# Optimization experiments

Measured on AMD Instinct MI355X. Metric: run time of the kernel, lower is better.

## Reference

```python
import jax, jax.numpy as jnp
import numpy as np

H = 128          # hidden
L = 4            # num PNA layers
NG = 32          # graphs in the batch
OUT = 12
N_NODES = 30000
N_EDGES = 480000
IN_NODE = 64
IN_EDGE = 16
EPS_BN = 1e-5
EPS_STD = 1e-5
# deg histogram torch.tensor([1,2,3,4,5,6]): cnt_i nodes have degree i
_cnt = np.arange(1.0, 7.0)
AVG_LOG = float((np.log(np.arange(6) + 1.0) * _cnt).sum() / _cnt.sum())


def _lin(k, fan_in, fan_out):
    return jax.random.normal(k, (fan_in, fan_out), jnp.float32) * 0.05


def setup_inputs() -> dict:
    key = jax.random.key(0)
    ks = jax.random.split(key, 16)
    d = {}
    d["x"] = jax.random.normal(ks[0], (N_NODES, IN_NODE), jnp.float32)
    d["edge_attr"] = jax.random.normal(ks[1], (N_EDGES, IN_EDGE), jnp.float32)
    d["edge_index"] = jax.random.randint(ks[2], (2, N_EDGES), 0, N_NODES)
    d["batch"] = jnp.sort(jax.random.randint(ks[3], (N_NODES,), 0, NG))
    d["node_emb_W"] = _lin(ks[4], IN_NODE, H)
    d["node_emb_b"] = jnp.zeros((H,), jnp.float32)
    d["edge_emb_W"] = _lin(ks[5], IN_EDGE, H)
    d["edge_emb_b"] = jnp.zeros((H,), jnp.float32)
    kl = jax.random.split(ks[6], 4 * L)
    d["edge_enc_W"] = jnp.stack([_lin(kl[i], H, H) for i in range(L)])
    d["edge_enc_b"] = jnp.zeros((L, H), jnp.float32)
    d["pre_W"] = jnp.stack([_lin(kl[L + i], 3 * H, H) for i in range(L)])
    d["pre_b"] = jnp.zeros((L, H), jnp.float32)
    d["post_W"] = jnp.stack([_lin(kl[2 * L + i], 13 * H, H) for i in range(L)])
    d["post_b"] = jnp.zeros((L, H), jnp.float32)
    d["lin_W"] = jnp.stack([_lin(kl[3 * L + i], H, H) for i in range(L)])
    d["lin_b"] = jnp.zeros((L, H), jnp.float32)
    d["bn_gamma"] = jnp.ones((L, H), jnp.float32)
    d["bn_beta"] = jnp.zeros((L, H), jnp.float32)
    d["head1_W"] = _lin(ks[7], H, H // 2)
    d["head1_b"] = jnp.zeros((H // 2,), jnp.float32)
    d["head2_W"] = _lin(ks[8], H // 2, OUT)
    d["head2_b"] = jnp.zeros((OUT,), jnp.float32)
    return d


def _pna_layer(x, e, src, dst, eW, eb, pW, pb, oW, ob, lW, lb):
    n = x.shape[0]
    ee = e @ eW + eb                                      # edge encoder [E, H]
    h = jnp.concatenate([x[dst], x[src], ee], axis=-1)    # (x_i, x_j, e) [E, 3H]
    m = h @ pW + pb                                       # pre-nn messages [E, H]
    ones = jnp.ones((m.shape[0],), m.dtype)
    deg = jax.ops.segment_sum(ones, dst, num_segments=n)  # in-degree [N]
    degc = jnp.maximum(deg, 1.0)[:, None]
    has = (deg > 0.0)[:, None]
    mean = jax.ops.segment_sum(m, dst, num_segments=n) / degc
    mn = jnp.where(has, jax.ops.segment_min(m, dst, num_segments=n), 0.0)
    mx = jnp.where(has, jax.ops.segment_max(m, dst, num_segments=n), 0.0)
    mean_sq = jax.ops.segment_sum(m * m, dst, num_segments=n) / degc
    std = jnp.sqrt(jax.nn.relu(mean_sq - mean * mean) + EPS_STD)
    agg = jnp.concatenate([mean, mn, mx, std], axis=-1)   # aggregators [N, 4H]
    amp = jnp.log(degc + 1.0) / AVG_LOG                   # amplification scale
    out = jnp.concatenate([agg, agg * amp, agg / amp], axis=-1)  # id/amp/atten [N, 12H]
    out = jnp.concatenate([x, out], axis=-1) @ oW + ob    # post-nn [N, H]
    return out @ lW + lb                                  # final lin


def reference(x, edge_index, batch, edge_attr, node_emb_W, node_emb_b,
              edge_emb_W, edge_emb_b, edge_enc_W, edge_enc_b, pre_W, pre_b,
              post_W, post_b, lin_W, lin_b, bn_gamma, bn_beta,
              head1_W, head1_b, head2_W, head2_b):
    src, dst = edge_index[0], edge_index[1]
    h = x @ node_emb_W + node_emb_b
    e = edge_attr @ edge_emb_W + edge_emb_b
    for l in range(L):
        h = _pna_layer(h, e, src, dst, edge_enc_W[l], edge_enc_b[l],
                       pre_W[l], pre_b[l], post_W[l], post_b[l],
                       lin_W[l], lin_b[l])
        mu = h.mean(axis=0)
        var = h.var(axis=0)  # biased, as BatchNorm training-mode normalization
        h = (h - mu) / jnp.sqrt(var + EPS_BN) * bn_gamma[l] + bn_beta[l]
        h = jax.nn.relu(h)   # dropout == identity (eval mode reference)
    g = jax.ops.segment_sum(h, batch, num_segments=NG)   # global_add_pool [NG, H]
    z = jax.nn.relu(g @ head1_W + head1_b)
    return z @ head2_W + head2_b
```

## Files before the change

kernel.cpp:

```cpp
#include <hip/hip_runtime.h>
#include <hip/hip_bf16.h>
#include <math.h>

#define NN 30000
#define NE 480000
#define NLAYER 4
#define NGR 32
#define NOUT 12
#define EPS_BN 1e-5f
#define EPS_STD 1e-5f
#define AVG_LOG 1.3821454785305053f
#define MB_GRID 235
#define MB2 469

typedef unsigned short ushort_t;
typedef __bf16 bf16x8 __attribute__((ext_vector_type(8)));
typedef float floatx4 __attribute__((ext_vector_type(4)));

__device__ __forceinline__ float bfu(ushort_t u){
  union { unsigned int ui; float f; } c; c.ui = ((unsigned int)u) << 16; return c.f;
}
__device__ __forceinline__ ushort_t f2bf(float f){
  union { float f; unsigned int u; } c; c.f = f;
  unsigned int lsb = (c.u >> 16) & 1u;
  c.u += 0x7FFFu + lsb;
  return (ushort_t)(c.u >> 16);
}

__device__ __forceinline__ int plausible(unsigned int bits32){
  unsigned int e = (bits32 >> 23) & 0xFF;
  if(e == 0xFF) return 0;
  if(bits32 == 0 || bits32 == 0x80000000u) return 1;
  return (e >= 93 && e <= 140) ? 1 : 0;
}

__global__ void k_detect(const ushort_t* __restrict__ xr, int* __restrict__ flag){
  __shared__ int cnt[2];
  if(threadIdx.x < 2) cnt[threadIdx.x] = 0;
  __syncthreads();
  const unsigned int* xf = (const unsigned int*)xr;
  int gf = 0, gb = 0;
  for(int i = threadIdx.x; i < 1024; i += 256){
    gf += plausible(xf[i]);
    gb += plausible(((unsigned int)xr[i]) << 16);
  }
  atomicAdd(&cnt[0], gf);
  atomicAdd(&cnt[1], gb);
  __syncthreads();
  if(threadIdx.x == 0) *flag = (cnt[1] >= cnt[0]) ? 1 : 0;
}

#define NJOBS 18
struct CvtJob { const void* s; float* d; int n; };
struct CvtArgs { CvtJob j[NJOBS]; const int* flag; };

__global__ void k_cvt(CvtArgs a){
  int ji = blockIdx.y;
  const int isbf = *a.flag;
  float* d = a.j[ji].d;
  int n = a.j[ji].n;
  if(isbf){
    const ushort_t* s = (const ushort_t*)a.j[ji].s;
    for(int i = blockIdx.x*256 + threadIdx.x; i < n; i += gridDim.x*256) d[i] = bfu(s[i]);
  } else {
    const float* s = (const float*)a.j[ji].s;
    for(int i = blockIdx.x*256 + threadIdx.x; i < n; i += gridDim.x*256) d[i] = s[i];
  }
}

__global__ void k_xbf(const void* __restrict__ x, ushort_t* __restrict__ d,
                      const int* __restrict__ flag){
  int i = blockIdx.x*256 + threadIdx.x;
  if(i >= NN*64) return;
  if(*flag) d[i] = ((const ushort_t*)x)[i];
  else      d[i] = f2bf(((const float*)x)[i]);
}

#define NTR 9
struct TrJob { const float* s; ushort_t* d; int K, N; };
struct TrArgs { TrJob j[NTR]; };

__global__ void k_tr(TrArgs a){
  TrJob j = a.j[blockIdx.y];
  int nk = j.K >> 6, nn = j.N >> 6;
  int tile = blockIdx.x;
  if(tile >= nk*nn) return;
  int tk = tile % nk, tn = tile / nk;
  int k0 = tk*64, n0 = tn*64;
  __shared__ float t[64][65];
  int w = threadIdx.x >> 6, c = threadIdx.x & 63;
  #pragma unroll
  for(int i=0;i<16;i+=1){
    int r = i*4 + w;
    t[r][c] = j.s[(size_t)(k0+r)*j.N + n0 + c];
  }
  __syncthreads();
  #pragma unroll
  for(int i=0;i<16;i+=1){
    int r = i*4 + w;
    j.d[(size_t)(n0+r)*j.K + k0 + c] = f2bf(t[c][r]);
  }
}

#define NFOLD 16
struct FoldJob { const float* s1; const float* s2; ushort_t* d; int Kd; };
struct FoldArgs { FoldJob j[NFOLD]; };

__global__ void k_fold(FoldArgs a){
  FoldJob j = a.j[blockIdx.y];
  const int n0 = blockIdx.x*16;
  __shared__ float s2s[128][16];
  int tid = threadIdx.x;
  for(int idx = tid; idx < 128*16; idx += 256){
    int t = idx >> 4, jj = idx & 15;
    s2s[t][jj] = j.s2[t*128 + n0 + jj];
  }
  __syncthreads();
  for(int k = tid; k < j.Kd; k += 256){
    float part[16];
    #pragma unroll
    for(int p=0;p<16;p++) part[p] = 0.f;
    for(int t0=0; t0<128; t0+=32){
      float rr[32];
      #pragma unroll
      for(int tt=0;tt<32;tt++) rr[tt] = j.s1[(size_t)k*128 + t0 + tt];
      #pragma unroll
      for(int p=0;p<16;p++){
        float acc = 0.f;
        #pragma unroll
        for(int tt=0;tt<32;tt++) acc += rr[tt]*s2s[t0+tt][p];
        part[p] += acc;
      }
    }
    #pragma unroll
    for(int p=0;p<16;p++)
      j.d[(size_t)(n0+p)*j.Kd + k] = f2bf(part[p]);
  }
}

__global__ void k_foldb(const float* __restrict__ postB, const float* __restrict__ linW,
                        const float* __restrict__ linB, float* __restrict__ biasY){
  int l = blockIdx.x, c = threadIdx.x;
  float a = linB[l*128+c];
  const float* L = linW + (size_t)l*128*128;
  const float* pb = postB + l*128;
  for(int t=0;t<128;t++) a += pb[t]*L[t*128+c];
  biasY[l*128+c] = a;
}

__global__ void k_deg(const int* __restrict__ dst, int* __restrict__ deg){
  int i = blockIdx.x*256 + threadIdx.x;
  if(i < NE){
    unsigned d = (unsigned)dst[i];
    if(d < NN) atomicAdd(&deg[d], 1);
  }
}

__global__ void k_scan1(const int* __restrict__ deg, int* __restrict__ rp,
                        int* __restrict__ bsum){
  __shared__ int wsum[16];
  int tid = threadIdx.x, lane = tid & 63, wid = tid >> 6;
  int i = blockIdx.x*1024 + tid;
  int v = (i < NN) ? deg[i] : 0;
  int incl = v;
  #pragma unroll
  for(int off=1; off<64; off<<=1){
    int t = __shfl_up(incl, off, 64);
    if(lane >= off) incl += t;
  }
  if(lane==63) wsum[wid] = incl;
  __syncthreads();
  int woff = 0;
  for(int w=0; w<wid; w++) woff += wsum[w];
  if(i < NN) rp[i+1] = incl + woff;
  if(tid == 0){
    int t = 0;
    for(int w=0; w<16; w++) t += wsum[w];
    bsum[blockIdx.x] = t;
  }
}

__global__ void k_scan2(const int* __restrict__ bsum, int* __restrict__ boff,
                        int* __restrict__ rp, int nb){
  if(threadIdx.x == 0){
    int run = 0;
    for(int b=0;b<nb;b++){ boff[b] = run; run += bsum[b]; }
    rp[0] = 0;
  }
}

__global__ void k_scan3(int* __restrict__ rp, const int* __restrict__ boff){
  int i = blockIdx.x*1024 + threadIdx.x;
  if(i < NN) rp[i+1] += boff[blockIdx.x];
}

__global__ void k_scatter(const int* __restrict__ dst,
                          const int* __restrict__ rp, int* __restrict__ fill,
                          int* __restrict__ eix_csr){
  int i = blockIdx.x*256 + threadIdx.x;
  if(i >= NE) return;
  unsigned d = (unsigned)dst[i];
  if(d >= NN) return;
  int pos = rp[d] + atomicAdd(&fill[d], 1);
  eix_csr[pos] = i;
}

__launch_bounds__(64)
__global__ void k_srt(const int* __restrict__ rp, int* __restrict__ eix){
  __shared__ int buf[64][129];
  int t = threadIdx.x;
  int n = blockIdx.x*64 + t;
  if(n >= NN) return;
  int s0 = rp[n], e0 = rp[n+1], d = e0 - s0;
  if(d <= 1) return;
  if(d <= 128){
    int* b = buf[t];
    for(int i=0;i<d;i++) b[i] = eix[s0+i];
    for(int i=1;i<d;i++){
      int k = b[i], j = i-1;
      while(j >= 0 && b[j] > k){ b[j+1] = b[j]; j--; }
      b[j+1] = k;
    }
    for(int i=0;i<d;i++) eix[s0+i] = b[i];
  } else {
    for(int i=s0+1;i<e0;i++){
      int k = eix[i], j = i-1;
      while(j >= s0 && eix[j] > k){ eix[j+1] = eix[j]; j--; }
      eix[j+1] = k;
    }
  }
}

__global__ void k_gather_ea(const int* __restrict__ eix, const int* __restrict__ esrc,
                            const void* __restrict__ ea,
                            ushort_t* __restrict__ out, int* __restrict__ src_csr,
                            const int* __restrict__ flag){
  int j = blockIdx.x*128 + threadIdx.x;
  if(j >= NE) return;
  int i = eix[j];
  src_csr[j] = esrc[i];
  uint4* d = (uint4*)(out + (size_t)j*16);
  if(*flag){
    const uint4* s = (const uint4*)((const ushort_t*)ea + (size_t)i*16);
    d[0] = s[0]; d[1] = s[1];
  } else {
    const float* s = (const float*)ea + (size_t)i*16;
    union { ushort_t us[16]; uint4 u4[2]; } pk;
    #pragma unroll
    for(int k=0;k<16;k++) pk.us[k] = f2bf(s[k]);
    d[0] = pk.u4[0]; d[1] = pk.u4[1];
  }
}

__global__ void k_prep_K(const float* __restrict__ embW, const float* __restrict__ embB,
                         const float* __restrict__ encW, const float* __restrict__ encB,
                         const float* __restrict__ preW, const float* __restrict__ preB,
                         float* __restrict__ Kf){
  int bx = blockIdx.x;
  int l = bx / 17, r = bx % 17;
  int c = threadIdx.x;
  const float* eW = encW + (size_t)l*128*128;
  const float* P3 = preW + (size_t)l*384*128 + 256*128;
  __shared__ float trow[128];
  float a;
  if(r < 16){
    a = 0.f;
    const float* w = embW + r*128;
    for(int k=0;k<128;k++) a += w[k]*eW[k*128+c];
  } else {
    a = encB[l*128+c];
    for(int k=0;k<128;k++) a += embB[k]*eW[k*128+c];
  }
  trow[c] = a;
  __syncthreads();
  float o = (r==16) ? preB[l*128+c] : 0.f;
  for(int k=0;k<128;k++) o += trow[k]*P3[k*128+c];
  Kf[(size_t)l*17*128 + r*128 + c] = o;
}

__global__ void k_prep_Kfrag(const float* __restrict__ Kf, ushort_t* __restrict__ KfT,
                             float* __restrict__ Kfb){
  int b = blockIdx.x;
  int l = b >> 3, t = b & 7;
  int lane = threadIdx.x;
  int quad = lane >> 4, l15 = lane & 15;
  const float* K = Kf + (size_t)l*17*128;
  ushort_t* o = KfT + (((size_t)l*8 + t)*64 + lane)*8;
  #pragma unroll
  for(int j=0;j<8;j++){
    int k = quad*8 + j;
    int col = t*16 + l15;
    o[j] = (k < 16) ? f2bf(K[k*128 + col]) : (ushort_t)0;
  }
  if(t == 0){
    Kfb[l*128 + lane]      = K[16*128 + lane];
    Kfb[l*128 + lane + 64] = K[16*128 + lane + 64];
  }
}

template<int EPI, int OUTBF>
__launch_bounds__(256)
__global__ void k_mm(const ushort_t* __restrict__ A, const ushort_t* __restrict__ BT,
                     void* __restrict__ C, void* __restrict__ C2,
                     int M, int K, int ldc, const float* __restrict__ bias){
  __shared__ __align__(16) ushort_t Als[128][88];
  __shared__ __align__(16) ushort_t Bls[128][88];
  const int tid = threadIdx.x;
  const int m0 = blockIdx.x*128, n0 = blockIdx.y*128;
  const int w = tid >> 6, lane = tid & 63;
  const int wm = (w & 1)*64, wn = (w >> 1)*64;
  const int quad = lane >> 4, l15 = lane & 15;
  floatx4 acc[4][4] = {};

  for(int k0=0; k0<K; k0+=64){
    #pragma unroll
    for(int i=0;i<4;i++){
      int c = tid + 256*i;
      int row = c >> 3, kc = (c & 7)*8;
      uint4 va = make_uint4(0u,0u,0u,0u);
      int gr = m0 + row;
      if(gr < M) va = *(const uint4*)(A + (size_t)gr*K + k0 + kc);
      *(uint4*)(&Als[row][kc]) = va;
      uint4 vb = *(const uint4*)(BT + (size_t)(n0+row)*K + k0 + kc);
      *(uint4*)(&Bls[row][kc]) = vb;
    }
    __syncthreads();
    #pragma unroll
    for(int ks=0; ks<64; ks+=32){
      bf16x8 a[4], b[4];
      #pragma unroll
      for(int i=0;i<4;i++) a[i] = *(const bf16x8*)(&Als[wm+16*i+l15][ks+quad*8]);
      #pragma unroll
      for(int j=0;j<4;j++) b[j] = *(const bf16x8*)(&Bls[wn+16*j+l15][ks+quad*8]);
      #pragma unroll
      for(int i=0;i<4;i++)
        #pragma unroll
        for(int j=0;j<4;j++)
          acc[i][j] = __builtin_amdgcn_mfma_f32_16x16x32_bf16(a[i], b[j], acc[i][j], 0, 0, 0);
    }
    __syncthreads();
  }

  #pragma unroll
  for(int i=0;i<4;i++){
    #pragma unroll
    for(int r=0;r<4;r++){
      int grow = m0 + wm + 16*i + quad*4 + r;
      if(grow >= M) continue;
      #pragma unroll
      for(int j=0;j<4;j++){
        int gcol = n0 + wn + 16*j + l15;
        float v = acc[i][j][r];
        if(EPI==0){
          if(bias) v += bias[gcol];
          if(OUTBF) ((ushort_t*)C)[(size_t)grow*ldc + gcol] = f2bf(v);
          else      ((float*)  C)[(size_t)grow*ldc + gcol] = v;
        } else {
          if(n0 == 0) ((float*)C)[(size_t)grow*128 + gcol] = v;
          else        ((ushort_t*)C2)[(size_t)grow*128 + (gcol-128)] = f2bf(v);
        }
      }
    }
  }
}

__launch_bounds__(256)
__global__ void k_post(const ushort_t* __restrict__ aggb, const ushort_t* __restrict__ h,
                       const ushort_t* __restrict__ Wcat, const ushort_t* __restrict__ W0,
                       const float* __restrict__ biasY,
                       const float* __restrict__ ampv, const float* __restrict__ invv,
                       ushort_t* __restrict__ y, float* __restrict__ bnpart){
  __shared__ __align__(16) ushort_t Als[64][88];
  __shared__ __align__(16) ushort_t Bls[128][88];
  __shared__ float s_part[4][128];
  __shared__ float q_part[4][128];
  __shared__ float amp_s[64];
  __shared__ float inv_s[64];
  const int tid = threadIdx.x;
  const int m0 = blockIdx.x*64;
  const int w = tid >> 6, lane = tid & 63;
  const int quad = lane >> 4, l15 = lane & 15;
  const int cw = w*32;
  if(tid < 64){
    int rr = min(m0 + tid, NN-1);
    amp_s[tid] = ampv[rr];
    inv_s[tid] = invv[rr];
  }
  floatx4 accY[4][2] = {};

  for(int p=0; p<3; p++){
    floatx4 accP[4][2] = {};
    floatx4 (*tgt)[2] = (p==0) ? accY : accP;
    const ushort_t* Wp = Wcat + (size_t)p*128*512;
    for(int k0=0; k0<512; k0+=64){
      #pragma unroll
      for(int i=0;i<2;i++){
        int c = tid + 256*i;
        int row = c >> 3, kc = (c & 7)*8;
        uint4 va = make_uint4(0u,0u,0u,0u);
        int gr = m0 + row;
        if(gr < NN) va = *(const uint4*)(aggb + (size_t)gr*512 + k0 + kc);
        *(uint4*)(&Als[row][kc]) = va;
      }
      #pragma unroll
      for(int i=0;i<4;i++){
        int c = tid + 256*i;
        int row = c >> 3, kc = (c & 7)*8;
        *(uint4*)(&Bls[row][kc]) = *(const uint4*)(Wp + (size_t)row*512 + k0 + kc);
      }
      __syncthreads();
      #pragma unroll
      for(int ks=0; ks<64; ks+=32){
        bf16x8 a[4], b[2];
        #pragma unroll
        for(int i=0;i<4;i++) a[i] = *(const bf16x8*)(&Als[16*i+l15][ks+quad*8]);
        #pragma unroll
        for(int j=0;j<2;j++) b[j] = *(const bf16x8*)(&Bls[cw+16*j+l15][ks+quad*8]);
        #pragma unroll
        for(int i=0;i<4;i++)
          #pragma unroll
          for(int j=0;j<2;j++)
            tgt[i][j] = __builtin_amdgcn_mfma_f32_16x16x32_bf16(a[i], b[j], tgt[i][j], 0, 0, 0);
      }
      __syncthreads();
    }
    if(p > 0){
      const float* cs = (p==1) ? amp_s : inv_s;
      #pragma unroll
      for(int i=0;i<4;i++)
        #pragma unroll
        for(int r=0;r<4;r++){
          float coef = cs[16*i + quad*4 + r];
          #pragma unroll
          for(int j=0;j<2;j++) accY[i][j][r] += coef*accP[i][j][r];
        }
    }
  }

  for(int k0=0; k0<128; k0+=64){
    #pragma unroll
    for(int i=0;i<2;i++){
      int c = tid + 256*i;
      int row = c >> 3, kc = (c & 7)*8;
      uint4 va = make_uint4(0u,0u,0u,0u);
      int gr = m0 + row;
      if(gr < NN) va = *(const uint4*)(h + (size_t)gr*128 + k0 + kc);
      *(uint4*)(&Als[row][kc]) = va;
    }
    #pragma unroll
    for(int i=0;i<4;i++){
      int c = tid + 256*i;
      int row = c >> 3, kc = (c & 7)*8;
      *(uint4*)(&Bls[row][kc]) = *(const uint4*)(W0 + (size_t)row*128 + k0 + kc);
    }
    __syncthreads();
    #pragma unroll
    for(int ks=0; ks<64; ks+=32){
      bf16x8 a[4], b[2];
      #pragma unroll
      for(int i=0;i<4;i++) a[i] = *(const bf16x8*)(&Als[16*i+l15][ks+quad*8]);
      #pragma unroll
      for(int j=0;j<2;j++) b[j] = *(const bf16x8*)(&Bls[cw+16*j+l15][ks+quad*8]);
      #pragma unroll
      for(int i=0;i<4;i++)
        #pragma unroll
        for(int j=0;j<2;j++)
          accY[i][j] = __builtin_amdgcn_mfma_f32_16x16x32_bf16(a[i], b[j], accY[i][j], 0, 0, 0);
    }
    __syncthreads();
  }

  float s[2] = {0,0}, q[2] = {0,0};
  #pragma unroll
  for(int i=0;i<4;i++){
    #pragma unroll
    for(int r=0;r<4;r++){
      int grow = m0 + 16*i + quad*4 + r;
      if(grow >= NN) continue;
      #pragma unroll
      for(int j=0;j<2;j++){
        int gcol = cw + 16*j + l15;
        float v = accY[i][j][r] + biasY[gcol];
        y[(size_t)grow*128 + gcol] = f2bf(v);
        s[j] += v; q[j] += v*v;
      }
    }
  }
  #pragma unroll
  for(int j=0;j<2;j++){
    s_part[quad][cw + 16*j + l15] = s[j];
    q_part[quad][cw + 16*j + l15] = q[j];
  }
  __syncthreads();
  if(tid < 128){
    float ss = 0.f, qq = 0.f;
    #pragma unroll
    for(int sl=0; sl<4; sl++){ ss += s_part[sl][tid]; qq += q_part[sl][tid]; }
    bnpart[(size_t)blockIdx.x*256 + tid]       = ss;
    bnpart[(size_t)blockIdx.x*256 + 128 + tid] = qq;
  }
}

__launch_bounds__(128)
__global__ void k_agg(const int* __restrict__ rp, const int* __restrict__ src_csr,
                      const ushort_t* __restrict__ ea_csr,
                      const ushort_t* __restrict__ KfT, const float* __restrict__ Kfb,
                      const float* __restrict__ Ah, const ushort_t* __restrict__ Bh,
                      ushort_t* __restrict__ agg, float* __restrict__ ampv,
                      float* __restrict__ invv){
  const int n = blockIdx.x, tid = threadIdx.x;
  const int wv = tid >> 6, lane = tid & 63;
  const int quad = lane >> 4, l15 = lane & 15;
  const int s0 = rp[n], e0 = rp[n+1], deg = e0 - s0;
  bf16x8 kf[4];
  float base[4];
  #pragma unroll
  for(int tt=0;tt<4;tt++){
    int t = wv*4 + tt;
    kf[tt] = *(const bf16x8*)(KfT + ((size_t)t*64 + lane)*8);
    int col = wv*64 + tt*16 + l15;
    base[tt] = Ah[(size_t)n*128 + col] + Kfb[col];
  }
  float sum[4], sq[4], mn[4], mx[4];
  #pragma unroll
  for(int tt=0;tt<4;tt++){ sum[tt]=0.f; sq[tt]=0.f; mn[tt]=INFINITY; mx[tt]=-INFINITY; }
  __shared__ __align__(16) ushort_t ea_s[16][16];
  __shared__ int src_s[16];

  for(int j0=s0; j0<e0; j0+=16){
    int cnt = min(16, e0-j0);
    __syncthreads();
    {
      int edge = tid >> 3, pos = (tid & 7)*2;
      int se = j0 + min(edge, cnt-1);
      *(unsigned int*)(&ea_s[edge][pos]) = *(const unsigned int*)(ea_csr + (size_t)se*16 + pos);
    }
    if(tid < 16) src_s[tid] = src_csr[min(j0+tid, e0-1)];
    __syncthreads();
    bf16x8 af = {};
    if(quad < 2) af = *(const bf16x8*)(&ea_s[l15][quad*8]);
    #pragma unroll
    for(int tt=0;tt<4;tt++){
      floatx4 zc = {0.f,0.f,0.f,0.f};
      floatx4 em = __builtin_amdgcn_mfma_f32_16x16x32_bf16(af, kf[tt], zc, 0, 0, 0);
      int col = wv*64 + tt*16 + l15;
      #pragma unroll
      for(int r=0;r<4;r++){
        int e = quad*4 + r;
        float bh = bfu(Bh[(size_t)src_s[e]*128 + col]);
        float m = base[tt] + bh + em[r];
        if(e < cnt){
          sum[tt] += m; sq[tt] += m*m;
          mn[tt] = fminf(mn[tt], m); mx[tt] = fmaxf(mx[tt], m);
        }
      }
    }
  }

  #pragma unroll
  for(int tt=0;tt<4;tt++){
    sum[tt] += __shfl_xor(sum[tt], 16); sum[tt] += __shfl_xor(sum[tt], 32);
    sq[tt]  += __shfl_xor(sq[tt], 16);  sq[tt]  += __shfl_xor(sq[tt], 32);
    mn[tt] = fminf(mn[tt], __shfl_xor(mn[tt], 16)); mn[tt] = fminf(mn[tt], __shfl_xor(mn[tt], 32));
    mx[tt] = fmaxf(mx[tt], __shfl_xor(mx[tt], 16)); mx[tt] = fmaxf(mx[tt], __shfl_xor(mx[tt], 32));
  }
  if(quad == 0){
    float degc = (float)(deg>0?deg:1);
    ushort_t* o = agg + (size_t)n*512;
    #pragma unroll
    for(int tt=0;tt<4;tt++){
      int col = wv*64 + tt*16 + l15;
      float mean = sum[tt]/degc;
      float var = fmaxf(sq[tt]/degc - mean*mean, 0.f);
      float sd = sqrtf(var + EPS_STD);
      float lmn = (deg==0) ? 0.f : mn[tt];
      float lmx = (deg==0) ? 0.f : mx[tt];
      o[col]       = f2bf(mean);
      o[128 + col] = f2bf(lmn);
      o[256 + col] = f2bf(lmx);
      o[384 + col] = f2bf(sd);
    }
  }
  if(tid == 0){
    float degc = (float)(deg>0?deg:1);
    float amp = logf(degc+1.f)/AVG_LOG;
    ampv[n] = amp; invv[n] = 1.f/amp;
  }
}

__global__ void k_bn_fin(const float* __restrict__ bnpart, int nb,
                         const float* __restrict__ gamma, const float* __restrict__ beta,
                         float* __restrict__ scale, float* __restrict__ shift){
  int c = threadIdx.x;
  float s0=0.f,s1=0.f,s2=0.f,s3=0.f, q0=0.f,q1=0.f,q2=0.f,q3=0.f;
  int b = 0;
  for(; b+3<nb; b+=4){
    s0 += bnpart[(size_t)(b+0)*256 + c];       q0 += bnpart[(size_t)(b+0)*256 + 128 + c];
    s1 += bnpart[(size_t)(b+1)*256 + c];       q1 += bnpart[(size_t)(b+1)*256 + 128 + c];
    s2 += bnpart[(size_t)(b+2)*256 + c];       q2 += bnpart[(size_t)(b+2)*256 + 128 + c];
    s3 += bnpart[(size_t)(b+3)*256 + c];       q3 += bnpart[(size_t)(b+3)*256 + 128 + c];
  }
  for(; b<nb; b++){ s0 += bnpart[(size_t)b*256 + c]; q0 += bnpart[(size_t)b*256 + 128 + c]; }
  float s = (s0+s1)+(s2+s3), q = (q0+q1)+(q2+q3);
  float mu  = s*(1.f/NN);
  float var = fmaxf(q*(1.f/NN) - mu*mu, 0.f);
  float inv = 1.f/sqrtf(var + EPS_BN);
  float sc = gamma[c]*inv;
  scale[c] = sc;
  shift[c] = beta[c] - mu*sc;
}

__global__ void k_bn_relu(const ushort_t* __restrict__ y, const float* __restrict__ scale,
                          const float* __restrict__ shift, ushort_t* __restrict__ h){
  int i = blockIdx.x*256 + threadIdx.x;
  if(i >= NN*128) return;
  int c = i & 127;
  float v = fmaxf(bfu(y[i])*scale[c] + shift[c], 0.f);
  h[i] = f2bf(v);
}

__device__ __forceinline__ int lbound(const int* a, int n, int v){
  int lo = 0, hi = n;
  while(lo < hi){ int mid = (lo+hi) >> 1; if(a[mid] < v) lo = mid+1; else hi = mid; }
  return lo;
}

__launch_bounds__(128)
__global__ void k_pool1(const ushort_t* __restrict__ h, const int* __restrict__ batch,
                        float* __restrict__ gpart){
  int b = blockIdx.x, ch = blockIdx.y, c = threadIdx.x;
  int lo = lbound(batch, NN, b), hi = lbound(batch, NN, b+1);
  int len = hi - lo;
  int per = (len + 7) >> 3;
  int r0 = min(lo + ch*per, hi);
  int r1 = min(r0 + per, hi);
  float acc = 0.f;
  for(int r=r0;r<r1;r++) acc += bfu(h[(size_t)r*128+c]);
  gpart[((size_t)b*8 + ch)*128 + c] = acc;
}

__global__ void k_pool2(const float* __restrict__ gpart, float* __restrict__ g){
  int b = blockIdx.x, c = threadIdx.x;
  float acc = 0.f;
  #pragma unroll
  for(int ch=0; ch<8; ch++) acc += gpart[((size_t)b*8 + ch)*128 + c];
  g[(size_t)b*128 + c] = acc;
}

__launch_bounds__(64)
__global__ void k_head(const float* __restrict__ g, const float* __restrict__ W1,
                       const float* __restrict__ b1, const float* __restrict__ W2,
                       const float* __restrict__ b2, void* __restrict__ out,
                       const int* __restrict__ flag){
  __shared__ float gs[128];
  __shared__ float zs[64];
  int r = blockIdx.x, tid = threadIdx.x;
  gs[tid] = g[r*128 + tid];
  gs[tid+64] = g[r*128 + tid + 64];
  __syncthreads();
  float a = b1[tid];
  for(int k=0;k<128;k++) a += gs[k]*W1[k*64+tid];
  zs[tid] = fmaxf(a, 0.f);
  __syncthreads();
  if(tid < NOUT){
    float o = b2[tid];
    for(int k=0;k<64;k++) o += zs[k]*W2[k*12+tid];
    if(*flag) ((ushort_t*)out)[r*NOUT + tid] = f2bf(o);
    else      ((float*)out)[r*NOUT + tid] = o;
  }
}

extern "C" void kernel_launch(void* const* d_in, const int* in_sizes, int n_in,
                              void* d_out, int out_size, void* d_ws, size_t ws_size,
                              hipStream_t stream){
  const void* x_raw = d_in[0];
  const void* ea_raw;
  const int*  eidx;
  const int*  batch;
  if(in_sizes[1] == 2*NE){
    eidx   = (const int*)d_in[1];
    batch  = (const int*)d_in[2];
    ea_raw = d_in[3];
  } else {
    ea_raw = d_in[1];
    eidx   = (const int*)d_in[2];
    batch  = (const int*)d_in[3];
  }
  const void* nembW_r = d_in[4];
  const void* nembB_r = d_in[5];
  const void* eembW_r = d_in[6];
  const void* eembB_r = d_in[7];
  const void* encW_r  = d_in[8];
  const void* encB_r  = d_in[9];
  const void* preW_r  = d_in[10];
  const void* preB_r  = d_in[11];
  const void* postW_r = d_in[12];
  const void* postB_r = d_in[13];
  const void* linW_r  = d_in[14];
  const void* linB_r  = d_in[15];
  const void* bnG_r   = d_in[16];
  const void* bnB_r   = d_in[17];
  const void* h1W_r   = d_in[18];
  const void* h1B_r   = d_in[19];
  const void* h2W_r   = d_in[20];
  const void* h2B_r   = d_in[21];

  char* p = (char*)d_ws;
  auto alloc = [&](size_t bytes)->void*{
    void* r = (void*)p; p += (bytes + 255) & ~(size_t)255; return r;
  };
  int*      dtflag  = (int*)     alloc(sizeof(int)*16);
  int*      deg     = (int*)     alloc(sizeof(int)*NN);
  int*      fill    = (int*)     alloc(sizeof(int)*NN);
  int*      rp      = (int*)     alloc(sizeof(int)*(NN+1));
  int*      bsum    = (int*)     alloc(sizeof(int)*64);
  int*      boff    = (int*)     alloc(sizeof(int)*64);
  int*      src_csr = (int*)     alloc(sizeof(int)*NE);
  int*      eix_csr = (int*)     alloc(sizeof(int)*NE);
  ushort_t* ea_csr  = (ushort_t*)alloc(sizeof(ushort_t)*(size_t)NE*16);
  ushort_t* xbf     = (ushort_t*)alloc(sizeof(ushort_t)*(size_t)NN*64);
  ushort_t* h       = (ushort_t*)alloc(sizeof(ushort_t)*(size_t)NN*128);
  ushort_t* aggb    = (ushort_t*)alloc(sizeof(ushort_t)*(size_t)NN*512);
  float*    Ah      = (float*)   alloc(sizeof(float)*(size_t)NN*128);
  ushort_t* Bh      = (ushort_t*)alloc(sizeof(ushort_t)*(size_t)NN*128);
  ushort_t* y       = (ushort_t*)alloc(sizeof(ushort_t)*(size_t)NN*128);
  float*    ampv    = (float*)   alloc(sizeof(float)*(NN+256));
  float*    invv    = (float*)   alloc(sizeof(float)*(NN+256));
  float*    Kf      = (float*)   alloc(sizeof(float)*4*17*128);
  ushort_t* KfTf    = (ushort_t*)alloc(sizeof(ushort_t)*4*8*64*8);
  float*    Kfb     = (float*)   alloc(sizeof(float)*4*128);
  float*    bnpart  = (float*)   alloc(sizeof(float)*(size_t)MB2*256);
  float*    bnscale = (float*)   alloc(sizeof(float)*128);
  float*    bnshift = (float*)   alloc(sizeof(float)*128);
  float*    gpart   = (float*)   alloc(sizeof(float)*32*8*128);
  float*    g       = (float*)   alloc(sizeof(float)*32*128);
  float*    biasY   = (float*)   alloc(sizeof(float)*4*128);
  ushort_t* WembT   = (ushort_t*)alloc(sizeof(ushort_t)*128*64);
  ushort_t* P12T    = (ushort_t*)alloc(sizeof(ushort_t)*4*256*128);
  ushort_t* WcatFT  = (ushort_t*)alloc(sizeof(ushort_t)*(size_t)4*384*512);
  ushort_t* W0FT    = (ushort_t*)alloc(sizeof(ushort_t)*4*128*128);
  float* nembW = (float*)alloc(sizeof(float)*64*128);
  float* nembB = (float*)alloc(sizeof(float)*128);
  float* eembW = (float*)alloc(sizeof(float)*16*128);
  float* eembB = (float*)alloc(sizeof(float)*128);
  float* encW  = (float*)alloc(sizeof(float)*4*128*128);
  float* encB  = (float*)alloc(sizeof(float)*4*128);
  float* preW  = (float*)alloc(sizeof(float)*4*384*128);
  float* preB  = (float*)alloc(sizeof(float)*4*128);
  float* postW = (float*)alloc(sizeof(float)*(size_t)4*1664*128);
  float* postB = (float*)alloc(sizeof(float)*4*128);
  float* linW  = (float*)alloc(sizeof(float)*4*128*128);
  float* linB  = (float*)alloc(sizeof(float)*4*128);
  float* bnG   = (float*)alloc(sizeof(float)*4*128);
  float* bnB   = (float*)alloc(sizeof(float)*4*128);
  float* h1W   = (float*)alloc(sizeof(float)*128*64);
  float* h1B   = (float*)alloc(sizeof(float)*64);
  float* h2W   = (float*)alloc(sizeof(float)*64*12);
  float* h2B   = (float*)alloc(sizeof(float)*12);

  CvtArgs ca;
  ca.flag = dtflag;
  int ji = 0;
  auto job = [&](const void* s, float* d, int n){ ca.j[ji].s=s; ca.j[ji].d=d; ca.j[ji].n=n; ji++; };
  job(nembW_r, nembW, 64*128);
  job(nembB_r, nembB, 128);
  job(eembW_r, eembW, 16*128);
  job(eembB_r, eembB, 128);
  job(encW_r,  encW,  4*128*128);
  job(encB_r,  encB,  4*128);
  job(preW_r,  preW,  4*384*128);
  job(preB_r,  preB,  4*128);
  job(postW_r, postW, 4*1664*128);
  job(postB_r, postB, 4*128);
  job(linW_r,  linW,  4*128*128);
  job(linB_r,  linB,  4*128);
  job(bnG_r,   bnG,   4*128);
  job(bnB_r,   bnB,   4*128);
  job(h1W_r,   h1W,   128*64);
  job(h1B_r,   h1B,   64);
  job(h2W_r,   h2W,   64*12);
  job(h2B_r,   h2B,   12);

  TrArgs ta;
  int ti = 0;
  auto tj = [&](const float* s, ushort_t* d, int K, int N){ ta.j[ti].s=s; ta.j[ti].d=d; ta.j[ti].K=K; ta.j[ti].N=N; ti++; };
  tj(nembW, WembT, 64, 128);
  for(int l=0;l<4;l++){
    const float* pw = preW + (size_t)l*384*128;
    tj(pw,           P12T + (size_t)l*256*128,           128, 128);
    tj(pw + 128*128, P12T + (size_t)l*256*128 + 128*128, 128, 128);
  }

  FoldArgs fa;
  int fi = 0;
  for(int l=0;l<4;l++){
    const float* po = postW + (size_t)l*1664*128;
    const float* L  = linW + (size_t)l*128*128;
    for(int b=0;b<3;b++){
      fa.j[fi].s1 = po + (size_t)(128 + b*512)*128;
      fa.j[fi].s2 = L;
      fa.j[fi].d  = WcatFT + (size_t)l*384*512 + (size_t)b*128*512;
      fa.j[fi].Kd = 512;
      fi++;
    }
    fa.j[fi].s1 = po;
    fa.j[fi].s2 = L;
    fa.j[fi].d  = W0FT + (size_t)l*128*128;
    fa.j[fi].Kd = 128;
    fi++;
  }

  const int* esrc = eidx;
  const int* edst = eidx + NE;

  hipMemsetAsync(deg, 0, sizeof(int)*NN, stream);
  hipMemsetAsync(fill, 0, sizeof(int)*NN, stream);

  k_detect<<<1, 256, 0, stream>>>((const ushort_t*)x_raw, dtflag);
  k_cvt<<<dim3(128, NJOBS), 256, 0, stream>>>(ca);
  k_xbf<<<(NN*64+255)/256, 256, 0, stream>>>(x_raw, xbf, dtflag);
  k_tr<<<dim3(4, NTR), 256, 0, stream>>>(ta);
  k_fold<<<dim3(8, NFOLD), 256, 0, stream>>>(fa);
  k_foldb<<<4, 128, 0, stream>>>(postB, linW, linB, biasY);
  k_prep_K<<<68, 128, 0, stream>>>(eembW, eembB, encW, encB, preW, preB, Kf);
  k_prep_Kfrag<<<32, 64, 0, stream>>>(Kf, KfTf, Kfb);

  k_deg<<<(NE+255)/256, 256, 0, stream>>>(edst, deg);
  k_scan1<<<30, 1024, 0, stream>>>(deg, rp, bsum);
  k_scan2<<<1, 64, 0, stream>>>(bsum, boff, rp, 30);
  k_scan3<<<30, 1024, 0, stream>>>(rp, boff);
  k_scatter<<<(NE+255)/256, 256, 0, stream>>>(edst, rp, fill, eix_csr);
  k_srt<<<(NN+63)/64, 64, 0, stream>>>(rp, eix_csr);
  k_gather_ea<<<(NE+127)/128, 128, 0, stream>>>(eix_csr, esrc, ea_raw, ea_csr, src_csr, dtflag);

  k_mm<0,1><<<dim3(MB_GRID,1), 256, 0, stream>>>(xbf, WembT, h, nullptr, NN, 64, 128, nembB);

  for(int l=0; l<NLAYER; l++){
    k_mm<2,0><<<dim3(MB_GRID,2), 256, 0, stream>>>(h, P12T + (size_t)l*256*128, Ah, Bh,
                                                   NN, 128, 128, nullptr);
    k_agg<<<NN, 128, 0, stream>>>(rp, src_csr, ea_csr,
                                  KfTf + (size_t)l*8*64*8, Kfb + l*128,
                                  Ah, Bh, aggb, ampv, invv);
    k_post<<<MB2, 256, 0, stream>>>(aggb, h, WcatFT + (size_t)l*384*512,
                                    W0FT + (size_t)l*128*128, biasY + l*128,
                                    ampv, invv, y, bnpart);
    k_bn_fin<<<1, 128, 0, stream>>>(bnpart, MB2, bnG + l*128, bnB + l*128,
                                    bnscale, bnshift);
    k_bn_relu<<<(NN*128+255)/256, 256, 0, stream>>>(y, bnscale, bnshift, h);
  }

  k_pool1<<<dim3(NGR,8), 128, 0, stream>>>(h, batch, gpart);
  k_pool2<<<NGR, 128, 0, stream>>>(gpart, g);
  k_head<<<NGR, 64, 0, stream>>>(g, h1W, h1B, h2W, h2B, d_out, dtflag);
}
```

Baseline: 1.054 ms.

## Precompute per-edge encoder messages in separate MFMA kernel, simplify aggregation

Adds a kernel that computes the per-edge projected edge features (edge_attr times folded weights) for all edges via MFMA and stores them as bf16 in a tiled layout. The aggregation kernel then becomes a simple per-column loop that reads the precomputed edge term, gathers Bh for the source node, and accumulates mean/min/max/std without shared memory or syncs. This removes the per-node MFMA and barrier overhead for low-degree nodes. In exchange it writes and re-reads a 480000x128 bf16 buffer each layer (about 123MB of write plus read traffic), adds a kernel launch per layer, and rounds the edge term to bf16 before accumulation.

```diff
diff --git a/kernel.cpp b/kernel.cpp
--- a/kernel.cpp
+++ b/kernel.cpp
@@ -16,6 +16,7 @@
 typedef unsigned short ushort_t;
 typedef __bf16 bf16x8 __attribute__((ext_vector_type(8)));
 typedef float floatx4 __attribute__((ext_vector_type(4)));
+typedef ushort_t u16x4 __attribute__((ext_vector_type(4)));
 
 __device__ __forceinline__ float bfu(ushort_t u){
   union { unsigned int ui; float f; } c; c.ui = ((unsigned int)u) << 16; return c.f;
@@ -295,6 +296,33 @@
   if(t == 0){
     Kfb[l*128 + lane]      = K[16*128 + lane];
     Kfb[l*128 + lane + 64] = K[16*128 + lane + 64];
+  }
+}
+
+__launch_bounds__(256)
+__global__ void k_em(const ushort_t* __restrict__ ea_csr, const ushort_t* __restrict__ KfT,
+                     ushort_t* __restrict__ Em){
+  const int tid = threadIdx.x;
+  const int wv = tid >> 6, lane = tid & 63;
+  const int quad = lane >> 4, l15 = lane & 15;
+  bf16x8 kf[8];
+  #pragma unroll
+  for(int t=0;t<8;t++) kf[t] = *(const bf16x8*)(KfT + ((size_t)t*64 + lane)*8);
+  #pragma unroll
+  for(int it=0; it<4; it++){
+    int ebase = blockIdx.x*256 + it*64 + wv*16;
+    bf16x8 af = {};
+    if(quad < 2)
+      af = *(const bf16x8*)(ea_csr + (size_t)(ebase + l15)*16 + quad*8);
+    ushort_t* tb = Em + (size_t)(ebase >> 4)*2048;
+    #pragma unroll
+    for(int t=0;t<8;t++){
+      floatx4 zc = {0.f,0.f,0.f,0.f};
+      floatx4 em = __builtin_amdgcn_mfma_f32_16x16x32_bf16(af, kf[t], zc, 0, 0, 0);
+      u16x4 pk;
+      pk.x = f2bf(em[0]); pk.y = f2bf(em[1]); pk.z = f2bf(em[2]); pk.w = f2bf(em[3]);
+      *(u16x4*)(tb + (size_t)(t*16 + l15)*16 + quad*4) = pk;
+    }
   }
 }
 
@@ -503,86 +531,32 @@
 
 __launch_bounds__(128)
 __global__ void k_agg(const int* __restrict__ rp, const int* __restrict__ src_csr,
-                      const ushort_t* __restrict__ ea_csr,
-                      const ushort_t* __restrict__ KfT, const float* __restrict__ Kfb,
+                      const ushort_t* __restrict__ Em, const float* __restrict__ Kfb,
                       const float* __restrict__ Ah, const ushort_t* __restrict__ Bh,
                       ushort_t* __restrict__ agg, float* __restrict__ ampv,
                       float* __restrict__ invv){
-  const int n = blockIdx.x, tid = threadIdx.x;
-  const int wv = tid >> 6, lane = tid & 63;
-  const int quad = lane >> 4, l15 = lane & 15;
+  const int n = blockIdx.x, c = threadIdx.x;
   const int s0 = rp[n], e0 = rp[n+1], deg = e0 - s0;
-  bf16x8 kf[4];
-  float base[4];
-  #pragma unroll
-  for(int tt=0;tt<4;tt++){
-    int t = wv*4 + tt;
-    kf[tt] = *(const bf16x8*)(KfT + ((size_t)t*64 + lane)*8);
-    int col = wv*64 + tt*16 + l15;
-    base[tt] = Ah[(size_t)n*128 + col] + Kfb[col];
-  }
-  float sum[4], sq[4], mn[4], mx[4];
-  #pragma unroll
-  for(int tt=0;tt<4;tt++){ sum[tt]=0.f; sq[tt]=0.f; mn[tt]=INFINITY; mx[tt]=-INFINITY; }
-  __shared__ __align__(16) ushort_t ea_s[16][16];
-  __shared__ int src_s[16];
-
-  for(int j0=s0; j0<e0; j0+=16){
-    int cnt = min(16, e0-j0);
-    __syncthreads();
-    {
-      int edge = tid >> 3, pos = (tid & 7)*2;
-      int se = j0 + min(edge, cnt-1);
-      *(unsigned int*)(&ea_s[edge][pos]) = *(const unsigned int*)(ea_csr + (size_t)se*16 + pos);
-    }
-    if(tid < 16) src_s[tid] = src_csr[min(j0+tid, e0-1)];
-    __syncthreads();
-    bf16x8 af = {};
-    if(quad < 2) af = *(const bf16x8*)(&ea_s[l15][quad*8]);
-    #pragma unroll
-    for(int tt=0;tt<4;tt++){
-      floatx4 zc = {0.f,0.f,0.f,0.f};
-      floatx4 em = __builtin_amdgcn_mfma_f32_16x16x32_bf16(af, kf[tt], zc, 0, 0, 0);
-      int col = wv*64 + tt*16 + l15;
-      #pragma unroll
-      for(int r=0;r<4;r++){
-        int e = quad*4 + r;
-        float bh = bfu(Bh[(size_t)src_s[e]*128 + col]);
-        float m = base[tt] + bh + em[r];
-        if(e < cnt){
-          sum[tt] += m; sq[tt] += m*m;
-          mn[tt] = fminf(mn[tt], m); mx[tt] = fmaxf(mx[tt], m);
-        }
-      }
-    }
-  }
-
-  #pragma unroll
-  for(int tt=0;tt<4;tt++){
-    sum[tt] += __shfl_xor(sum[tt], 16); sum[tt] += __shfl_xor(sum[tt], 32);
-    sq[tt]  += __shfl_xor(sq[tt], 16);  sq[tt]  += __shfl_xor(sq[tt], 32);
-    mn[tt] = fminf(mn[tt], __shfl_xor(mn[tt], 16)); mn[tt] = fminf(mn[tt], __shfl_xor(mn[tt], 32));
-    mx[tt] = fmaxf(mx[tt], __shfl_xor(mx[tt], 16)); mx[tt] = fmaxf(mx[tt], __shfl_xor(mx[tt], 32));
-  }
-  if(quad == 0){
-    float degc = (float)(deg>0?deg:1);
-    ushort_t* o = agg + (size_t)n*512;
-    #pragma unroll
-    for(int tt=0;tt<4;tt++){
-      int col = wv*64 + tt*16 + l15;
-      float mean = sum[tt]/degc;
-      float var = fmaxf(sq[tt]/degc - mean*mean, 0.f);
-      float sd = sqrtf(var + EPS_STD);
-      float lmn = (deg==0) ? 0.f : mn[tt];
-      float lmx = (deg==0) ? 0.f : mx[tt];
-      o[col]       = f2bf(mean);
-      o[128 + col] = f2bf(lmn);
-      o[256 + col] = f2bf(lmx);
-      o[384 + col] = f2bf(sd);
-    }
-  }
-  if(tid == 0){
-    float degc = (float)(deg>0?deg:1);
+  const float base = Ah[(size_t)n*128 + c] + Kfb[c];
+  float sum=0.f, sq=0.f, mn=INFINITY, mx=-INFINITY;
+  const int c16 = c << 4;
+  for(int j=s0; j<e0; j++){
+    int src = src_csr[j];
+    float m = base + bfu(Bh[(size_t)src*128 + c])
+                   + bfu(Em[((size_t)(j >> 4) << 11) + c16 + (j & 15)]);
+    sum += m; sq += m*m; mn = fminf(mn, m); mx = fmaxf(mx, m);
+  }
+  float degc = (float)(deg>0?deg:1);
+  float mean = sum/degc;
+  float var  = fmaxf(sq/degc - mean*mean, 0.f);
+  float sd = sqrtf(var + EPS_STD);
+  if(deg==0){ mn=0.f; mx=0.f; }
+  ushort_t* o = agg + (size_t)n*512;
+  o[c]     = f2bf(mean);
+  o[128+c] = f2bf(mn);
+  o[256+c] = f2bf(mx);
+  o[384+c] = f2bf(sd);
+  if(c==0){
     float amp = logf(degc+1.f)/AVG_LOG;
     ampv[n] = amp; invv[n] = 1.f/amp;
   }
@@ -718,6 +692,7 @@
   int*      src_csr = (int*)     alloc(sizeof(int)*NE);
   int*      eix_csr = (int*)     alloc(sizeof(int)*NE);
   ushort_t* ea_csr  = (ushort_t*)alloc(sizeof(ushort_t)*(size_t)NE*16);
+  ushort_t* Em      = (ushort_t*)alloc(sizeof(ushort_t)*(size_t)NE*128);
   ushort_t* xbf     = (ushort_t*)alloc(sizeof(ushort_t)*(size_t)NN*64);
   ushort_t* h       = (ushort_t*)alloc(sizeof(ushort_t)*(size_t)NN*128);
   ushort_t* aggb    = (ushort_t*)alloc(sizeof(ushort_t)*(size_t)NN*512);
@@ -836,10 +811,10 @@
   k_mm<0,1><<<dim3(MB_GRID,1), 256, 0, stream>>>(xbf, WembT, h, nullptr, NN, 64, 128, nembB);
 
   for(int l=0; l<NLAYER; l++){
+    k_em<<<NE/256, 256, 0, stream>>>(ea_csr, KfTf + (size_t)l*8*64*8, Em);
     k_mm<2,0><<<dim3(MB_GRID,2), 256, 0, stream>>>(h, P12T + (size_t)l*256*128, Ah, Bh,
                                                    NN, 128, 128, nullptr);
-    k_agg<<<NN, 128, 0, stream>>>(rp, src_csr, ea_csr,
-                                  KfTf + (size_t)l*8*64*8, Kfb + l*128,
+    k_agg<<<NN, 128, 0, stream>>>(rp, src_csr, Em, Kfb + l*128,
                                   Ah, Bh, aggb, ampv, invv);
     k_post<<<MB2, 256, 0, stream>>>(aggb, h, WcatFT + (size_t)l*384*512,
                                     W0FT + (size_t)l*128*128, biasY + l*128,
```

Result: slower. 1.269 ms (+20.5%).
